# Kernel tuning notes

Hardware: AMD Instinct MI355X
Metric: run time of the kernel (lower is better)

## Reference

```python
import jax, jax.numpy as jnp
import numpy as np

N, E, NB, P = 100000, 1600000, 1000, 500000


def gcn_conv(x, edge_index, W, b):
    # PyG GCNConv: add self-loops, symmetric D^-1/2 (A+I) D^-1/2 normalization,
    # linear transform, bias.
    n = x.shape[0]
    loop = jnp.arange(n, dtype=edge_index.dtype)
    src = jnp.concatenate([edge_index[0], loop])
    dst = jnp.concatenate([edge_index[1], loop])
    deg = jax.ops.segment_sum(jnp.ones(src.shape[0], x.dtype), dst, num_segments=n)
    dinv = jnp.where(deg > 0, jax.lax.rsqrt(deg), 0.0)
    norm = dinv[src] * dinv[dst]                       # [E+n]
    xw = x @ W                                          # [n, out]
    out = jax.ops.segment_sum(xw[src] * norm[:, None], dst, num_segments=n)
    return out + b


def setup_inputs() -> dict:
    key = jax.random.key(0)
    ks = jax.random.split(key, 12)
    x = jax.random.normal(ks[0], (N, 27), jnp.float32)
    edge_index = jax.random.randint(ks[1], (2, E), 0, N, dtype=jnp.int32)
    bank = jax.random.normal(ks[2], (NB, 27), jnp.float32)
    node1 = jax.random.randint(ks[3], (P,), 0, N + NB, dtype=jnp.int32)
    node2 = jax.random.randint(ks[4], (P,), 0, N + NB, dtype=jnp.int32)

    def lin(k, fan_in, fan_out):
        s = 1.0 / np.sqrt(fan_in)
        kw, kb = jax.random.split(k)
        W = jax.random.uniform(kw, (fan_in, fan_out), jnp.float32, -s, s)
        b = jax.random.uniform(kb, (fan_out,), jnp.float32, -s, s)
        return W, b

    W1, b1 = lin(ks[5], 27, 60)
    W2, b2 = lin(ks[6], 60, 50)
    Wb, bb = lin(ks[7], 27, 50)
    Wf1, bf1 = lin(ks[8], 100, 40)
    Wf2, bf2 = lin(ks[9], 40, 20)
    Wf3, bf3 = lin(ks[10], 20, 4)
    return dict(x=x, bank=bank, W1=W1, b1=b1, W2=W2, b2=b2, Wb=Wb, bb=bb,
                Wf1=Wf1, bf1=bf1, Wf2=Wf2, bf2=bf2, Wf3=Wf3, bf3=bf3,
                edge_index=edge_index, node1=node1, node2=node2)


def reference(x, bank, W1, b1, W2, b2, Wb, bb, Wf1, bf1, Wf2, bf2, Wf3, bf3,
              edge_index, node1, node2):
    h = gcn_conv(x, edge_index, W1, b1)                 # [N, 60]
    h = gcn_conv(h, edge_index, W2, b2)                 # [N, 50]
    bk = bank @ Wb + bb                                 # [NB, 50]
    allh = jnp.concatenate([h, bk], axis=0)             # [N+NB, 50]
    z = jnp.concatenate([allh[node1], allh[node2]], axis=1)  # [P, 100]
    z = z @ Wf1 + bf1
    z = z @ Wf2 + bf2
    z = z @ Wf3 + bf3                                   # [P, 4]
    return jax.nn.softmax(z, axis=0)                    # softmax over dim 0, as in source
```

## Files before the change

kernel.cpp:

```cpp
#include <hip/hip_runtime.h>
#include <math.h>

#define N_NODES 100000
#define N_EDGES 1600000
#define NB_BANK 1000
#define N_PAIRS 500000

#define BUCK_SHIFT 9
#define BUCK_NODES 512
#define NBUCK 196
#define BCAP 10240
#define EPB 16384
#define NSCAT 98
#define NZBLK 1954
#define SMASK 0x1FFFF

struct Consts {
  float C[27*8];
  float Rb[27*8];
  float u[8];
  float vg[8];
  float vb[8];
};

__device__ void precompute_body(
    const float* __restrict__ W1, const float* __restrict__ b1,
    const float* __restrict__ W2, const float* __restrict__ b2,
    const float* __restrict__ Wb, const float* __restrict__ bb,
    const float* __restrict__ Wf1, const float* __restrict__ bf1,
    const float* __restrict__ Wf2, const float* __restrict__ bf2,
    const float* __restrict__ Wf3, const float* __restrict__ bf3,
    Consts* __restrict__ cst) {
  __shared__ float A[40*4];
  __shared__ float T[100*4];
  __shared__ float B[60*8];
  __shared__ float cvec[4];
  const int tid = threadIdx.x;
  const int nt = blockDim.x;

  for (int idx = tid; idx < 160; idx += nt) {
    int r = idx >> 2, k = idx & 3;
    float s = 0.f;
    for (int j = 0; j < 20; ++j) s += Wf2[r*20+j] * Wf3[j*4+k];
    A[idx] = s;
  }
  __syncthreads();
  for (int idx = tid; idx < 400; idx += nt) {
    int r = idx >> 2, k = idx & 3;
    float s = 0.f;
    for (int j = 0; j < 40; ++j) s += Wf1[r*40+j] * A[j*4+k];
    T[idx] = s;
  }
  if (tid < 4) {
    float s = bf3[tid];
    for (int j = 0; j < 40; ++j) s += bf1[j] * A[j*4+tid];
    for (int j = 0; j < 20; ++j) s += bf2[j] * Wf3[j*4+tid];
    cvec[tid] = s;
  }
  __syncthreads();
  for (int idx = tid; idx < 480; idx += nt) {
    int r = idx >> 3, k = idx & 7;
    int half = k >> 2, kk = k & 3;
    float s = 0.f;
    for (int j = 0; j < 50; ++j) s += W2[r*50+j] * T[(half*50+j)*4+kk];
    B[idx] = s;
  }
  __syncthreads();
  for (int idx = tid; idx < 456; idx += nt) {
    if (idx < 216) {
      int r = idx >> 3, k = idx & 7;
      float s = 0.f;
      for (int j = 0; j < 60; ++j) s += W1[r*60+j] * B[j*8+k];
      cst->C[idx] = s;
    } else if (idx < 432) {
      int i2 = idx - 216;
      int r = i2 >> 3, k = i2 & 7, half = k >> 2, kk = k & 3;
      float s = 0.f;
      for (int j = 0; j < 50; ++j) s += Wb[r*50+j] * T[(half*50+j)*4+kk];
      cst->Rb[i2] = s;
    } else if (idx < 440) {
      int k = idx - 432;
      float s = 0.f;
      for (int j = 0; j < 60; ++j) s += b1[j] * B[j*8+k];
      cst->u[k] = s;
    } else if (idx < 448) {
      int k = idx - 440, half = k >> 2, kk = k & 3;
      float s = (half == 0) ? cvec[kk] : 0.f;
      for (int j = 0; j < 50; ++j) s += b2[j] * T[(half*50+j)*4+kk];
      cst->vg[k] = s;
    } else {
      int k = idx - 448, half = k >> 2, kk = k & 3;
      float s = (half == 0) ? cvec[kk] : 0.f;
      for (int j = 0; j < 50; ++j) s += bb[j] * T[(half*50+j)*4+kk];
      cst->vb[k] = s;
    }
  }
}

__global__ __launch_bounds__(1024) void k_scatter(
    const int* __restrict__ ei, int* __restrict__ bcnt, int* __restrict__ ebuf,
    const float* __restrict__ W1, const float* __restrict__ b1,
    const float* __restrict__ W2, const float* __restrict__ b2,
    const float* __restrict__ Wb, const float* __restrict__ bb,
    const float* __restrict__ Wf1, const float* __restrict__ bf1,
    const float* __restrict__ Wf2, const float* __restrict__ bf2,
    const float* __restrict__ Wf3, const float* __restrict__ bf3,
    Consts* __restrict__ cst) {
  if (blockIdx.x == NSCAT) {
    precompute_body(W1, b1, W2, b2, Wb, bb, Wf1, bf1, Wf2, bf2, Wf3, bf3, cst);
    return;
  }
  __shared__ int hist[NBUCK];
  __shared__ int base[NBUCK];
  const int t = threadIdx.x;
  const int e0 = blockIdx.x * EPB;
  if (t < NBUCK) hist[t] = 0;
  __syncthreads();
  for (int i = t; i < EPB; i += 1024) {
    int e = e0 + i;
    if (e < N_EDGES) atomicAdd(&hist[ei[N_EDGES + e] >> BUCK_SHIFT], 1);
  }
  __syncthreads();
  if (t < NBUCK) {
    int h = hist[t];
    base[t] = h ? (t * BCAP + atomicAdd(&bcnt[t], h)) : 0;
    hist[t] = 0;
  }
  __syncthreads();
  for (int i = t; i < EPB; i += 1024) {
    int e = e0 + i;
    if (e < N_EDGES) {
      int s = ei[e], d = ei[N_EDGES + e];
      int b = d >> BUCK_SHIFT;
      int pos = base[b] + atomicAdd(&hist[b], 1);
      ebuf[pos] = ((d & (BUCK_NODES - 1)) << 17) | s;
    }
  }
}

__global__ __launch_bounds__(512) void k_degfill(const int* __restrict__ bcnt,
                                                 const int* __restrict__ ebuf,
                                                 float* __restrict__ dinv,
                                                 int* __restrict__ rbeg,
                                                 int* __restrict__ rend,
                                                 int* __restrict__ csr) {
  __shared__ int cnt[BUCK_NODES];
  __shared__ int lcur[BUCK_NODES];
  const int b = blockIdx.x;
  const int t = threadIdx.x;
  cnt[t] = 0;
  __syncthreads();
  const int beg = b * BCAP, end = beg + bcnt[b];
  for (int j = beg + t; j < end; j += 512)
    atomicAdd(&cnt[ebuf[j] >> 17], 1);
  __syncthreads();
  int v = cnt[t];
  for (int off = 1; off < 512; off <<= 1) {
    int u = (t >= off) ? cnt[t - off] : 0;
    __syncthreads();
    cnt[t] += u;
    __syncthreads();
  }
  const int node = (b << BUCK_SHIFT) + t;
  const int excl = beg + cnt[t] - v;
  lcur[t] = excl;
  if (node < N_NODES) {
    rbeg[node] = excl;
    rend[node] = excl + v;
    dinv[node] = rsqrtf((float)v + 1.0f);
  }
  __syncthreads();
  for (int j = beg + t; j < end; j += 512) {
    int code = ebuf[j];
    int pos = atomicAdd(&lcur[code >> 17], 1);
    csr[pos] = code & SMASK;
  }
}

__global__ __launch_bounds__(256) void k_x8(const float* __restrict__ x,
                                            const float* __restrict__ dinv,
                                            const Consts* __restrict__ cst,
                                            float* __restrict__ Xs) {
  __shared__ float xs[32*27];
  const int tid = threadIdx.x;
  const int base = blockIdx.x * 32 * 27;
  for (int j = tid; j < 32*27; j += 256) {
    int g = base + j;
    xs[j] = (g < N_NODES*27) ? x[g] : 0.f;
  }
  __syncthreads();
  int li = tid >> 3, k = tid & 7;
  int node = blockIdx.x * 32 + li;
  if (node < N_NODES) {
    float s = 0.f;
    for (int c = 0; c < 27; ++c) s += xs[li*27+c] * cst->C[c*8+k];
    Xs[node*8+k] = s * dinv[node];
  }
}

__global__ __launch_bounds__(256) void k_gather1(const int* __restrict__ rbeg,
                                                 const int* __restrict__ rend,
                                                 const int* __restrict__ csr,
                                                 const float* __restrict__ dinv,
                                                 const float2* __restrict__ Xs2,
                                                 float2* __restrict__ Ys2,
                                                 float* __restrict__ dvec) {
  int t = blockIdx.x * 256 + threadIdx.x;
  int d = t >> 2, q = t & 3;
  if (d >= N_NODES) return;
  const int beg = rbeg[d], end = rend[d];
  const float nd = dinv[d];
  float2 self = Xs2[d*4 + q];
  float ax = self.x, ay = self.y;
  float dsum = nd;
  int j = beg;
  for (; j + 4 <= end; j += 4) {
    int s0 = csr[j], s1 = csr[j+1], s2 = csr[j+2], s3 = csr[j+3];
    float2 a0 = Xs2[s0*4+q], a1 = Xs2[s1*4+q], a2 = Xs2[s2*4+q], a3 = Xs2[s3*4+q];
    ax += (a0.x + a1.x) + (a2.x + a3.x);
    ay += (a0.y + a1.y) + (a2.y + a3.y);
    if (q == 0) dsum += (dinv[s0] + dinv[s1]) + (dinv[s2] + dinv[s3]);
  }
  for (; j < end; ++j) {
    int s = csr[j];
    float2 a = Xs2[s*4+q];
    ax += a.x; ay += a.y;
    if (q == 0) dsum += dinv[s];
  }
  float nn = nd * nd;
  Ys2[t] = make_float2(nn * ax, nn * ay);
  if (q == 0) dvec[d] = nd * dsum;
}

__global__ __launch_bounds__(256) void k_gather2g(const int* __restrict__ rbeg,
                                                  const int* __restrict__ rend,
                                                  const int* __restrict__ csr,
                                                  const float* __restrict__ dinv,
                                                  const float2* __restrict__ Ys2,
                                                  const float* __restrict__ dvec,
                                                  const float* __restrict__ bank,
                                                  const Consts* __restrict__ cst,
                                                  float2* __restrict__ gall2) {
  int t = blockIdx.x * 256 + threadIdx.x;
  int d = t >> 2, q = t & 3;
  if (d >= N_NODES + NB_BANK) return;
  int c0 = 2*q, c1 = 2*q + 1;
  if (d >= N_NODES) {
    int bk = d - N_NODES;
    float sx = cst->vb[c0], sy = cst->vb[c1];
    for (int cc = 0; cc < 27; ++cc) {
      float bv = bank[bk*27+cc];
      sx += bv * cst->Rb[cc*8+c0];
      sy += bv * cst->Rb[cc*8+c1];
    }
    gall2[t] = make_float2(sx, sy);
    return;
  }
  const int beg = rbeg[d], end = rend[d];
  float2 self = Ys2[d*4 + q];
  float ax = self.x, ay = self.y;
  int j = beg;
  for (; j + 4 <= end; j += 4) {
    int s0 = csr[j], s1 = csr[j+1], s2 = csr[j+2], s3 = csr[j+3];
    float2 a0 = Ys2[s0*4+q], a1 = Ys2[s1*4+q], a2 = Ys2[s2*4+q], a3 = Ys2[s3*4+q];
    ax += (a0.x + a1.x) + (a2.x + a3.x);
    ay += (a0.y + a1.y) + (a2.y + a3.y);
  }
  for (; j < end; ++j) {
    float2 a = Ys2[csr[j]*4+q];
    ax += a.x; ay += a.y;
  }
  float nd = dinv[d], dv = dvec[d];
  gall2[t] = make_float2(nd * ax + dv * cst->u[c0] + cst->vg[c0],
                         nd * ay + dv * cst->u[c1] + cst->vg[c1]);
}

__device__ inline void sm_merge(float4& m1, float4& s1,
                                const float4 m2, const float4 s2) {
  float4 M;
  M.x = fmaxf(m1.x, m2.x); M.y = fmaxf(m1.y, m2.y);
  M.z = fmaxf(m1.z, m2.z); M.w = fmaxf(m1.w, m2.w);
  s1.x = s1.x * expf(m1.x - M.x) + s2.x * expf(m2.x - M.x);
  s1.y = s1.y * expf(m1.y - M.y) + s2.y * expf(m2.y - M.y);
  s1.z = s1.z * expf(m1.z - M.z) + s2.z * expf(m2.z - M.z);
  s1.w = s1.w * expf(m1.w - M.w) + s2.w * expf(m2.w - M.w);
  m1 = M;
}

__global__ __launch_bounds__(256) void k_z(const int* __restrict__ node1,
                                           const int* __restrict__ node2,
                                           const float* __restrict__ gall,
                                           float* __restrict__ z,
                                           float4* __restrict__ bs_m,
                                           float4* __restrict__ bs_s) {
  int p = blockIdx.x * 256 + threadIdx.x;
  float4 m = make_float4(-1e30f, -1e30f, -1e30f, -1e30f);
  float4 s = make_float4(0.f, 0.f, 0.f, 0.f);
  if (p < N_PAIRS) {
    int n1 = node1[p], n2 = node2[p];
    const float4 a = *(const float4*)(gall + (size_t)n1*8);
    const float4 b = *(const float4*)(gall + (size_t)n2*8 + 4);
    float4 zv = make_float4(a.x+b.x, a.y+b.y, a.z+b.z, a.w+b.w);
    ((float4*)z)[p] = zv;
    m = zv; s = make_float4(1.f, 1.f, 1.f, 1.f);
  }
  __shared__ float4 lm[256], ls[256];
  lm[threadIdx.x] = m; ls[threadIdx.x] = s;
  __syncthreads();
  for (int st = 128; st > 0; st >>= 1) {
    if (threadIdx.x < st) {
      float4 mm = lm[threadIdx.x], ss = ls[threadIdx.x];
      sm_merge(mm, ss, lm[threadIdx.x + st], ls[threadIdx.x + st]);
      lm[threadIdx.x] = mm; ls[threadIdx.x] = ss;
    }
    __syncthreads();
  }
  if (threadIdx.x == 0) { bs_m[blockIdx.x] = lm[0]; bs_s[blockIdx.x] = ls[0]; }
}

__global__ __launch_bounds__(256) void k_comb(const float4* __restrict__ bs_m,
                                              const float4* __restrict__ bs_s,
                                              float* __restrict__ gms) {
  float4 m = make_float4(-1e30f, -1e30f, -1e30f, -1e30f);
  float4 s = make_float4(0.f, 0.f, 0.f, 0.f);
  for (int i = threadIdx.x; i < NZBLK; i += 256)
    sm_merge(m, s, bs_m[i], bs_s[i]);
  __shared__ float4 lm[256], ls[256];
  lm[threadIdx.x] = m; ls[threadIdx.x] = s;
  __syncthreads();
  for (int st = 128; st > 0; st >>= 1) {
    if (threadIdx.x < st) {
      float4 mm = lm[threadIdx.x], ss = ls[threadIdx.x];
      sm_merge(mm, ss, lm[threadIdx.x + st], ls[threadIdx.x + st]);
      lm[threadIdx.x] = mm; ls[threadIdx.x] = ss;
    }
    __syncthreads();
  }
  if (threadIdx.x == 0) {
    float4 M = lm[0], S = ls[0];
    gms[0] = M.x; gms[1] = M.y; gms[2] = M.z; gms[3] = M.w;
    gms[4] = S.x; gms[5] = S.y; gms[6] = S.z; gms[7] = S.w;
  }
}

__global__ __launch_bounds__(256) void k_final(const float* __restrict__ z,
                                               const float* __restrict__ gms,
                                               float* __restrict__ out) {
  int p = blockIdx.x * 256 + threadIdx.x;
  if (p < N_PAIRS) {
    float m0 = gms[0], m1 = gms[1], m2 = gms[2], m3 = gms[3];
    float i0 = 1.f / gms[4], i1 = 1.f / gms[5];
    float i2 = 1.f / gms[6], i3 = 1.f / gms[7];
    float4 zv = ((const float4*)z)[p];
    float4 o = make_float4(expf(zv.x - m0) * i0, expf(zv.y - m1) * i1,
                           expf(zv.z - m2) * i2, expf(zv.w - m3) * i3);
    ((float4*)out)[p] = o;
  }
}

extern "C" void kernel_launch(void* const* d_in, const int* in_sizes, int n_in,
                              void* d_out, int out_size, void* d_ws, size_t ws_size,
                              hipStream_t stream) {
  const float* x    = (const float*)d_in[0];
  const float* bank = (const float*)d_in[1];
  const float* W1   = (const float*)d_in[2];
  const float* b1   = (const float*)d_in[3];
  const float* W2   = (const float*)d_in[4];
  const float* b2   = (const float*)d_in[5];
  const float* Wb   = (const float*)d_in[6];
  const float* bb   = (const float*)d_in[7];
  const float* Wf1  = (const float*)d_in[8];
  const float* bf1  = (const float*)d_in[9];
  const float* Wf2  = (const float*)d_in[10];
  const float* bf2  = (const float*)d_in[11];
  const float* Wf3  = (const float*)d_in[12];
  const float* bf3  = (const float*)d_in[13];
  const int* ei     = (const int*)d_in[14];
  const int* node1  = (const int*)d_in[15];
  const int* node2  = (const int*)d_in[16];
  float* out = (float*)d_out;

  char* w = (char*)d_ws;
  size_t off = 0;
  auto take = [&](size_t bytes) -> char* {
    char* p = w + off;
    off = (off + bytes + 255) & ~(size_t)255;
    return p;
  };
  Consts* cst    = (Consts*)take(sizeof(Consts));
  int*    bcnt   = (int*)take(NBUCK * 4);
  float*  dinv   = (float*)take(N_NODES * 4);
  int*    rbeg   = (int*)take(N_NODES * 4);
  int*    rend   = (int*)take(N_NODES * 4);
  int*    csr    = (int*)take((size_t)NBUCK * BCAP * 4);
  float*  Xs     = (float*)take((size_t)N_NODES * 8 * 4);
  float*  Ys     = (float*)take((size_t)N_NODES * 8 * 4);
  float*  dvec   = (float*)take(N_NODES * 4);
  float*  gall   = (float*)take((size_t)(N_NODES + NB_BANK) * 8 * 4);
  char*   shreg  = take((size_t)NBUCK * BCAP * 4 > (size_t)N_PAIRS * 16
                        ? (size_t)NBUCK * BCAP * 4 : (size_t)N_PAIRS * 16);
  int*    ebuf   = (int*)shreg;
  float*  z      = (float*)shreg;
  float4* bs_m   = (float4*)take((size_t)NZBLK * 16);
  float4* bs_s   = (float4*)take((size_t)NZBLK * 16);
  float*  gms    = (float*)take(32);

  hipMemsetAsync(bcnt, 0, NBUCK * 4, stream);

  k_scatter<<<NSCAT + 1, 1024, 0, stream>>>(ei, bcnt, ebuf, W1, b1, W2, b2,
                                            Wb, bb, Wf1, bf1, Wf2, bf2,
                                            Wf3, bf3, cst);
  k_degfill<<<NBUCK, 512, 0, stream>>>(bcnt, ebuf, dinv, rbeg, rend, csr);
  k_x8<<<(N_NODES + 31) / 32, 256, 0, stream>>>(x, dinv, cst, Xs);
  k_gather1<<<(N_NODES * 4 + 255) / 256, 256, 0, stream>>>(
      rbeg, rend, csr, dinv, (const float2*)Xs, (float2*)Ys, dvec);
  k_gather2g<<<((N_NODES + NB_BANK) * 4 + 255) / 256, 256, 0, stream>>>(
      rbeg, rend, csr, dinv, (const float2*)Ys, dvec, bank, cst, (float2*)gall);
  k_z<<<NZBLK, 256, 0, stream>>>(node1, node2, gall, z, bs_m, bs_s);
  k_comb<<<1, 256, 0, stream>>>(bs_m, bs_s, gms);
  k_final<<<NZBLK, 256, 0, stream>>>(z, gms, out);
}
```

Baseline: 209.5 us.

## Fuse softmax combine into final pass, recompute z, cache dst in scatter

Removes the intermediate z buffer and the single-block combine kernel. Each final block redoes the reduction of per-block max/sum partials and recomputes z from gall via the node indices. Scatter keeps destination indices in registers instead of reloading them. Degfill uses 1024 threads per block. This saves a launch and the z write/read, but adds a redundant reduction over about 2K partials in every final block plus repeated gathers.

```diff
diff --git a/kernel.cpp b/kernel.cpp
--- a/kernel.cpp
+++ b/kernel.cpp
@@ -114,11 +114,15 @@
   __shared__ int base[NBUCK];
   const int t = threadIdx.x;
   const int e0 = blockIdx.x * EPB;
+  int dcache[EPB / 1024];
   if (t < NBUCK) hist[t] = 0;
   __syncthreads();
-  for (int i = t; i < EPB; i += 1024) {
-    int e = e0 + i;
-    if (e < N_EDGES) atomicAdd(&hist[ei[N_EDGES + e] >> BUCK_SHIFT], 1);
+#pragma unroll
+  for (int i = 0; i < EPB / 1024; ++i) {
+    int e = e0 + i * 1024 + t;
+    int d = (e < N_EDGES) ? ei[N_EDGES + e] : -1;
+    dcache[i] = d;
+    if (d >= 0) atomicAdd(&hist[d >> BUCK_SHIFT], 1);
   }
   __syncthreads();
   if (t < NBUCK) {
@@ -127,10 +131,12 @@
     hist[t] = 0;
   }
   __syncthreads();
-  for (int i = t; i < EPB; i += 1024) {
-    int e = e0 + i;
-    if (e < N_EDGES) {
-      int s = ei[e], d = ei[N_EDGES + e];
+#pragma unroll
+  for (int i = 0; i < EPB / 1024; ++i) {
+    int e = e0 + i * 1024 + t;
+    int d = dcache[i];
+    if (d >= 0) {
+      int s = ei[e];
       int b = d >> BUCK_SHIFT;
       int pos = base[b] + atomicAdd(&hist[b], 1);
       ebuf[pos] = ((d & (BUCK_NODES - 1)) << 17) | s;
@@ -138,39 +144,41 @@
   }
 }
 
-__global__ __launch_bounds__(512) void k_degfill(const int* __restrict__ bcnt,
-                                                 const int* __restrict__ ebuf,
-                                                 float* __restrict__ dinv,
-                                                 int* __restrict__ rbeg,
-                                                 int* __restrict__ rend,
-                                                 int* __restrict__ csr) {
+__global__ __launch_bounds__(1024) void k_degfill(const int* __restrict__ bcnt,
+                                                  const int* __restrict__ ebuf,
+                                                  float* __restrict__ dinv,
+                                                  int* __restrict__ rbeg,
+                                                  int* __restrict__ rend,
+                                                  int* __restrict__ csr) {
   __shared__ int cnt[BUCK_NODES];
   __shared__ int lcur[BUCK_NODES];
   const int b = blockIdx.x;
   const int t = threadIdx.x;
-  cnt[t] = 0;
+  if (t < BUCK_NODES) cnt[t] = 0;
   __syncthreads();
   const int beg = b * BCAP, end = beg + bcnt[b];
-  for (int j = beg + t; j < end; j += 512)
+  for (int j = beg + t; j < end; j += 1024)
     atomicAdd(&cnt[ebuf[j] >> 17], 1);
   __syncthreads();
-  int v = cnt[t];
-  for (int off = 1; off < 512; off <<= 1) {
-    int u = (t >= off) ? cnt[t - off] : 0;
+  int v = (t < BUCK_NODES) ? cnt[t] : 0;
+  for (int off = 1; off < BUCK_NODES; off <<= 1) {
+    int u = (t < BUCK_NODES && t >= off) ? cnt[t - off] : 0;
     __syncthreads();
-    cnt[t] += u;
+    if (t < BUCK_NODES) cnt[t] += u;
     __syncthreads();
   }
-  const int node = (b << BUCK_SHIFT) + t;
-  const int excl = beg + cnt[t] - v;
-  lcur[t] = excl;
-  if (node < N_NODES) {
-    rbeg[node] = excl;
-    rend[node] = excl + v;
-    dinv[node] = rsqrtf((float)v + 1.0f);
-  }
-  __syncthreads();
-  for (int j = beg + t; j < end; j += 512) {
+  if (t < BUCK_NODES) {
+    const int node = (b << BUCK_SHIFT) + t;
+    const int excl = beg + cnt[t] - v;
+    lcur[t] = excl;
+    if (node < N_NODES) {
+      rbeg[node] = excl;
+      rend[node] = excl + v;
+      dinv[node] = rsqrtf((float)v + 1.0f);
+    }
+  }
+  __syncthreads();
+  for (int j = beg + t; j < end; j += 1024) {
     int code = ebuf[j];
     int pos = atomicAdd(&lcur[code >> 17], 1);
     csr[pos] = code & SMASK;
@@ -287,22 +295,26 @@
   m1 = M;
 }
 
-__global__ __launch_bounds__(256) void k_z(const int* __restrict__ node1,
-                                           const int* __restrict__ node2,
-                                           const float* __restrict__ gall,
-                                           float* __restrict__ z,
-                                           float4* __restrict__ bs_m,
-                                           float4* __restrict__ bs_s) {
+__device__ inline float4 compute_z(int p, const int* __restrict__ node1,
+                                   const int* __restrict__ node2,
+                                   const float* __restrict__ gall) {
+  int n1 = node1[p], n2 = node2[p];
+  const float4 a = *(const float4*)(gall + (size_t)n1*8);
+  const float4 b = *(const float4*)(gall + (size_t)n2*8 + 4);
+  return make_float4(a.x+b.x, a.y+b.y, a.z+b.z, a.w+b.w);
+}
+
+__global__ __launch_bounds__(256) void k_zstats(const int* __restrict__ node1,
+                                                const int* __restrict__ node2,
+                                                const float* __restrict__ gall,
+                                                float4* __restrict__ bs_m,
+                                                float4* __restrict__ bs_s) {
   int p = blockIdx.x * 256 + threadIdx.x;
   float4 m = make_float4(-1e30f, -1e30f, -1e30f, -1e30f);
   float4 s = make_float4(0.f, 0.f, 0.f, 0.f);
   if (p < N_PAIRS) {
-    int n1 = node1[p], n2 = node2[p];
-    const float4 a = *(const float4*)(gall + (size_t)n1*8);
-    const float4 b = *(const float4*)(gall + (size_t)n2*8 + 4);
-    float4 zv = make_float4(a.x+b.x, a.y+b.y, a.z+b.z, a.w+b.w);
-    ((float4*)z)[p] = zv;
-    m = zv; s = make_float4(1.f, 1.f, 1.f, 1.f);
+    m = compute_z(p, node1, node2, gall);
+    s = make_float4(1.f, 1.f, 1.f, 1.f);
   }
   __shared__ float4 lm[256], ls[256];
   lm[threadIdx.x] = m; ls[threadIdx.x] = s;
@@ -318,9 +330,12 @@
   if (threadIdx.x == 0) { bs_m[blockIdx.x] = lm[0]; bs_s[blockIdx.x] = ls[0]; }
 }
 
-__global__ __launch_bounds__(256) void k_comb(const float4* __restrict__ bs_m,
-                                              const float4* __restrict__ bs_s,
-                                              float* __restrict__ gms) {
+__global__ __launch_bounds__(256) void k_final(const int* __restrict__ node1,
+                                               const int* __restrict__ node2,
+                                               const float* __restrict__ gall,
+                                               const float4* __restrict__ bs_m,
+                                               const float4* __restrict__ bs_s,
+                                               float* __restrict__ out) {
   float4 m = make_float4(-1e30f, -1e30f, -1e30f, -1e30f);
   float4 s = make_float4(0.f, 0.f, 0.f, 0.f);
   for (int i = threadIdx.x; i < NZBLK; i += 256)
@@ -336,24 +351,12 @@
     }
     __syncthreads();
   }
-  if (threadIdx.x == 0) {
-    float4 M = lm[0], S = ls[0];
-    gms[0] = M.x; gms[1] = M.y; gms[2] = M.z; gms[3] = M.w;
-    gms[4] = S.x; gms[5] = S.y; gms[6] = S.z; gms[7] = S.w;
-  }
-}
-
-__global__ __launch_bounds__(256) void k_final(const float* __restrict__ z,
-                                               const float* __restrict__ gms,
-                                               float* __restrict__ out) {
+  const float4 M = lm[0], S = ls[0];
   int p = blockIdx.x * 256 + threadIdx.x;
   if (p < N_PAIRS) {
-    float m0 = gms[0], m1 = gms[1], m2 = gms[2], m3 = gms[3];
-    float i0 = 1.f / gms[4], i1 = 1.f / gms[5];
-    float i2 = 1.f / gms[6], i3 = 1.f / gms[7];
-    float4 zv = ((const float4*)z)[p];
-    float4 o = make_float4(expf(zv.x - m0) * i0, expf(zv.y - m1) * i1,
-                           expf(zv.z - m2) * i2, expf(zv.w - m3) * i3);
+    float4 zv = compute_z(p, node1, node2, gall);
+    float4 o = make_float4(expf(zv.x - M.x) / S.x, expf(zv.y - M.y) / S.y,
+                           expf(zv.z - M.z) / S.z, expf(zv.w - M.w) / S.w);
     ((float4*)out)[p] = o;
   }
 }
@@ -397,26 +400,21 @@
   float*  Ys     = (float*)take((size_t)N_NODES * 8 * 4);
   float*  dvec   = (float*)take(N_NODES * 4);
   float*  gall   = (float*)take((size_t)(N_NODES + NB_BANK) * 8 * 4);
-  char*   shreg  = take((size_t)NBUCK * BCAP * 4 > (size_t)N_PAIRS * 16
-                        ? (size_t)NBUCK * BCAP * 4 : (size_t)N_PAIRS * 16);
-  int*    ebuf   = (int*)shreg;
-  float*  z      = (float*)shreg;
+  int*    ebuf   = (int*)take((size_t)NBUCK * BCAP * 4);
   float4* bs_m   = (float4*)take((size_t)NZBLK * 16);
   float4* bs_s   = (float4*)take((size_t)NZBLK * 16);
-  float*  gms    = (float*)take(32);
 
   hipMemsetAsync(bcnt, 0, NBUCK * 4, stream);
 
   k_scatter<<<NSCAT + 1, 1024, 0, stream>>>(ei, bcnt, ebuf, W1, b1, W2, b2,
                                             Wb, bb, Wf1, bf1, Wf2, bf2,
                                             Wf3, bf3, cst);
-  k_degfill<<<NBUCK, 512, 0, stream>>>(bcnt, ebuf, dinv, rbeg, rend, csr);
+  k_degfill<<<NBUCK, 1024, 0, stream>>>(bcnt, ebuf, dinv, rbeg, rend, csr);
   k_x8<<<(N_NODES + 31) / 32, 256, 0, stream>>>(x, dinv, cst, Xs);
   k_gather1<<<(N_NODES * 4 + 255) / 256, 256, 0, stream>>>(
       rbeg, rend, csr, dinv, (const float2*)Xs, (float2*)Ys, dvec);
   k_gather2g<<<((N_NODES + NB_BANK) * 4 + 255) / 256, 256, 0, stream>>>(
       rbeg, rend, csr, dinv, (const float2*)Ys, dvec, bank, cst, (float2*)gall);
-  k_z<<<NZBLK, 256, 0, stream>>>(node1, node2, gall, z, bs_m, bs_s);
-  k_comb<<<1, 256, 0, stream>>>(bs_m, bs_s, gms);
-  k_final<<<NZBLK, 256, 0, stream>>>(z, gms, out);
-}
+  k_zstats<<<NZBLK, 256, 0, stream>>>(node1, node2, gall, bs_m, bs_s);
+  k_final<<<NZBLK, 256, 0, stream>>>(node1, node2, gall, bs_m, bs_s, out);
+}
```

New measurement: 219.3 us. 1.05x slower.
